# Kernel tuning notes

Measured on AMD Instinct MI355X. Metric: run time of the kernel, lower is better.

## Reference

```python
import jax, jax.numpy as jnp
import numpy as np
from jax import lax

B_SZ, SEQ, D_MODEL, D_STATE, DT_RANK = 4, 4096, 256, 16, 16


def setup_inputs() -> dict:
    key = jax.random.key(0)
    ks = jax.random.split(key, 12)
    d, n, r = D_MODEL, D_STATE, DT_RANK
    inp = {}
    inp["hidden_states"] = jax.random.normal(ks[0], (B_SZ, SEQ, d), jnp.float32)
    inp["in_proj_w"] = jax.random.normal(ks[1], (3 * d, d), jnp.float32) * (d ** -0.5)
    inp["x_proj_w"] = jax.random.normal(ks[2], (r + 2 * n, d), jnp.float32) * (d ** -0.5)
    s = r ** -0.5
    inp["dt_proj_w"] = jax.random.uniform(ks[3], (d, r), jnp.float32, -s, s)
    dt = jnp.exp(jax.random.uniform(ks[4], (d,), jnp.float32) * (np.log(0.1) - np.log(1e-3)) + np.log(1e-3))
    inp["dt_proj_b"] = dt + jnp.log(-jnp.expm1(-dt))  # inverse-softplus init
    inp["A_log"] = jnp.log(jnp.broadcast_to(jnp.arange(1, n + 1, dtype=jnp.float32), (d, n)))
    inp["D"] = jnp.ones((d,), jnp.float32)
    inp["out_proj1_w"] = jax.random.normal(ks[5], (d, d), jnp.float32) * (d ** -0.5)
    inp["conv_x_w"] = jax.random.normal(ks[6], (d, 1, 1), jnp.float32)
    inp["conv_x_b"] = jax.random.normal(ks[7], (d,), jnp.float32) * 0.1
    inp["conv_y_w"] = jax.random.normal(ks[8], (d, 1, 3), jnp.float32) * (3 ** -0.5)
    inp["conv_y_b"] = jax.random.normal(ks[9], (d,), jnp.float32) * 0.1
    inp["conv_z_w"] = jax.random.normal(ks[10], (d, 1, 5), jnp.float32) * (5 ** -0.5)
    inp["conv_z_b"] = jax.random.normal(ks[11], (d,), jnp.float32) * 0.1
    return inp


def _silu(x):
    return x * jax.nn.sigmoid(x)


def _dwconv(x, w, b):
    # x: (b, d, l); w: (d, 1, k) depthwise; 'same' padding (odd k)
    k = w.shape[-1]
    pad = (k - 1) // 2
    out = lax.conv_general_dilated(
        x, w, window_strides=(1,), padding=[(pad, pad)],
        dimension_numbers=("NCH", "OIH", "NCH"), feature_group_count=x.shape[1])
    return out + b[None, :, None]


def _selective_scan(u, delta, A, B, C, D, delta_bias):
    # u, delta: (b,d,l); A: (d,n); B,C: (b,n,l); D, delta_bias: (d,)
    delta = jax.nn.softplus(delta + delta_bias[None, :, None])
    dA = jnp.exp(jnp.einsum("bdl,dn->lbdn", delta, A))          # (l,b,d,n)
    dBu = jnp.einsum("bdl,bnl,bdl->lbdn", delta, B, u)           # (l,b,d,n)
    Ct = jnp.transpose(C, (2, 0, 1))                             # (l,b,n)

    def step(h, inp):
        dA_t, dBu_t, C_t = inp
        h = dA_t * h + dBu_t                                     # (b,d,n)
        y = jnp.einsum("bdn,bn->bd", h, C_t)
        return h, y

    h0 = jnp.zeros(u.shape[:2] + (A.shape[1],), u.dtype)
    _, ys = lax.scan(step, h0, (dA, dBu, Ct))                    # ys: (l,b,d)
    y = jnp.transpose(ys, (1, 2, 0))                             # (b,d,l)
    return y + D[None, :, None] * u


def reference(hidden_states, in_proj_w, x_proj_w, dt_proj_w, dt_proj_b, A_log, D,
              out_proj1_w, conv_x_w, conv_x_b, conv_y_w, conv_y_b, conv_z_w, conv_z_b):
    b, l, d = hidden_states.shape
    xyz = jnp.einsum("ble,de->bdl", hidden_states, in_proj_w)    # (b, 3d, l)
    x, y, z = jnp.split(xyz, 3, axis=1)                          # each (b,d,l)
    A = -jnp.exp(A_log.astype(jnp.float32))
    x = _silu(_dwconv(x, conv_x_w, conv_x_b))
    y = _silu(_dwconv(y, conv_y_w, conv_y_b))
    z = _silu(_dwconv(z, conv_z_w, conv_z_b))
    x_dbl = jnp.einsum("bdl,ed->ble", x, x_proj_w)               # (b,l,r+2n)
    dt_r, Bm, Cm = jnp.split(x_dbl, [DT_RANK, DT_RANK + D_STATE], axis=-1)
    # dt_proj applies bias here; selective_scan adds delta_bias again (faithful to source)
    dt = jnp.einsum("blr,dr->bdl", dt_r, dt_proj_w) + dt_proj_b[None, :, None]
    Bm = jnp.transpose(Bm, (0, 2, 1))                            # (b,n,l)
    Cm = jnp.transpose(Cm, (0, 2, 1))
    p = _selective_scan(x, dt, A, Bm, Cm, D.astype(jnp.float32), dt_proj_b.astype(jnp.float32))
    p = jnp.transpose(p, (0, 2, 1))                              # (b,l,d)
    y = jnp.transpose(y, (0, 2, 1))
    z = jnp.transpose(z, (0, 2, 1))
    l1 = jnp.einsum("bld,ed->ble", p * y, out_proj1_w)
    l2 = l1 * z
    l2 = _dwconv(jnp.transpose(l2, (0, 2, 1)), conv_x_w, conv_x_b)
    return jnp.transpose(l2, (0, 2, 1))                          # (b,l,d)
```

## Files before the change

kernel.cpp:

```cpp
#include <hip/hip_runtime.h>
#include <hip/hip_bf16.h>
#include <math.h>

typedef __hip_bfloat16 bf16;
typedef __attribute__((ext_vector_type(8))) short bf16x8;
typedef __attribute__((ext_vector_type(4))) float f32x4;

#define B_SZ 4
#define SEQ  4096
#define DM   256
#define NST  16
#define NCHK 64
#define LC   (SEQ/NCHK)
#define MT   (B_SZ*SEQ)
#define CT   4
#define NLIN (B_SZ*16*256)

__device__ __forceinline__ float silu_f(float v){ return v / (1.f + __expf(-v)); }
__device__ __forceinline__ float softplus_f(float v){
  return (v > 15.f) ? v : __logf(1.f + __expf(v));
}
__device__ __forceinline__ short f2bf(float f){
  union { bf16 h; short s; } u; u.h = __float2bfloat16(f); return u.s;
}
__device__ __forceinline__ float bf2f(short s){
  union { unsigned int i; float f; } v;
  v.i = ((unsigned int)(unsigned short)s) << 16; return v.f;
}
__device__ __forceinline__ float4 bf4_to_f4(uint2 q){
  float4 f;
  f.x = bf2f((short)(q.x & 0xffffu)); f.y = bf2f((short)(q.x >> 16));
  f.z = bf2f((short)(q.y & 0xffffu)); f.w = bf2f((short)(q.y >> 16));
  return f;
}
__device__ __forceinline__ short4 f4_to_bf4(float4 f){
  short4 s; s.x = f2bf(f.x); s.y = f2bf(f.y); s.z = f2bf(f.z); s.w = f2bf(f.w);
  return s;
}

__device__ __forceinline__ void async_cp16(const short* g, short* l){
  __builtin_amdgcn_global_load_lds(
      (const __attribute__((address_space(1))) unsigned int*)g,
      (__attribute__((address_space(3))) unsigned int*)l, 16, 0, 0);
}

template<int CTRL>
__device__ __forceinline__ float dpp_add_step(float v){
  int x = __builtin_amdgcn_update_dpp(0, __float_as_int(v), CTRL, 0xf, 0xf, true);
  return v + __int_as_float(x);
}

__global__ __launch_bounds__(256)
void cvt_in_k(const float* __restrict__ w_in, const float* __restrict__ w_o1,
              const float* __restrict__ hs,
              short* __restrict__ w_in_b, short* __restrict__ w_o1_b,
              short* __restrict__ hsb)
{
  int i = blockIdx.x * 256 + threadIdx.x;
  if (i < 49152) {
    float4 q = *(const float4*)&w_in[i * 4];
    *(short4*)&w_in_b[i * 4] = f4_to_bf4(q);
  } else if (i < 65536) {
    int j = i - 49152;
    float4 q = *(const float4*)&w_o1[j * 4];
    *(short4*)&w_o1_b[j * 4] = f4_to_bf4(q);
  } else {
    int j = i - 65536;
    float4 q = *(const float4*)&hs[(size_t)j * 4];
    *(short4*)&hsb[(size_t)j * 4] = f4_to_bf4(q);
  }
}

template<int EPI, bool OBF, int BM>
__global__ __launch_bounds__(256)
void mfma_gemm_k(const short* __restrict__ Av, const short* __restrict__ Bw,
                 void* __restrict__ Outv, int N, int K,
                 const float* __restrict__ bias, const short* __restrict__ zc,
                 const float* __restrict__ cwx)
{
  constexpr int BN = 128, BK = 64;
  constexpr int JF = (BM == 64) ? 2 : 4;
  __shared__ short As[BM * BK];
  __shared__ short Bs[BN * BK];
  const int tid  = threadIdx.x;
  const int wave = tid >> 6, lane = tid & 63;
  const int quad = lane >> 4, l16 = lane & 15;
  const int wm = (BM == 64) ? 0 : (wave & 1) * 64;
  const int wn = (BM == 64) ? wave * 32 : (wave >> 1) * 64;
  const int m0 = blockIdx.x * BM, n0 = blockIdx.y * BN;

  f32x4 acc[4][JF] = {};

  for (int k0 = 0; k0 < K; k0 += BK) {
    #pragma unroll
    for (int p = 0; p < BM * 8 / 256; p++) {
      int id = p * 256 + tid;
      int row = id >> 3, slot = id & 7;
      int gch = slot ^ (row & 7);
      async_cp16(Av + (size_t)(m0 + row) * K + k0 + gch * 8,
                 &As[row * 64 + slot * 8]);
    }
    #pragma unroll
    for (int p = 0; p < 4; p++) {
      int id = p * 256 + tid;
      int row = id >> 3, slot = id & 7;
      int gch = slot ^ (row & 7);
      async_cp16(Bw + (size_t)(n0 + row) * K + k0 + gch * 8,
                 &Bs[row * 64 + slot * 8]);
    }
    __syncthreads();
    #pragma unroll
    for (int ks = 0; ks < 2; ks++) {
      bf16x8 fa[4], fb[JF];
      int sa = (ks * 4 + quad) ^ (l16 & 7);
      #pragma unroll
      for (int i = 0; i < 4; i++)
        fa[i] = *(const bf16x8*)&As[(wm + i * 16 + l16) * 64 + sa * 8];
      #pragma unroll
      for (int j = 0; j < JF; j++)
        fb[j] = *(const bf16x8*)&Bs[(wn + j * 16 + l16) * 64 + sa * 8];
      #pragma unroll
      for (int i = 0; i < 4; i++)
        #pragma unroll
        for (int j = 0; j < JF; j++)
          acc[i][j] = __builtin_amdgcn_mfma_f32_16x16x32_bf16(fa[i], fb[j], acc[i][j], 0, 0, 0);
    }
    __syncthreads();
  }

  #pragma unroll
  for (int i = 0; i < 4; i++) {
    #pragma unroll
    for (int j = 0; j < JF; j++) {
      int n = n0 + wn + j * 16 + l16;
      #pragma unroll
      for (int r = 0; r < 4; r++) {
        int m = m0 + wm + i * 16 + quad * 4 + r;
        float v = acc[i][j][r];
        if constexpr (EPI == 2)
          v = v * bf2f(zc[(size_t)m * N + n]) * cwx[n] + bias[n];
        if constexpr (OBF) ((short*)Outv)[(size_t)m * N + n] = f2bf(v);
        else               ((float*)Outv)[(size_t)m * N + n] = v;
      }
    }
  }
}

__global__ __launch_bounds__(256)
void gemm34_k(const short* __restrict__ xcb,
              const float* __restrict__ Bw,
              const float* __restrict__ wdt,
              const float* __restrict__ bdt,
              float* __restrict__ xdbl,
              float* __restrict__ dtv)
{
  constexpr int TM = 32, TK = 16, NN = 48;
  __shared__ __align__(16) float As[TK][TM + 4];
  __shared__ __align__(16) float Bs[TK][64 + 4];
  __shared__ __align__(16) float dt_s[TM][20];
  __shared__ __align__(16) float wdt_s[256][20];
  const int tid = threadIdx.x;
  const int tn = tid & 15, tm = tid >> 4;
  const int m0 = blockIdx.x * TM;
  float acc[2][4] = {};
  const int mlA = tid >> 3, kdA = (tid & 7) * 2;
  const int mlB = tid >> 2, kqB = (tid & 3) * 4;

  {
    float4 q0 = *(const float4*)&wdt[tid * 16 + 0];
    float4 q1 = *(const float4*)&wdt[tid * 16 + 4];
    float4 q2 = *(const float4*)&wdt[tid * 16 + 8];
    float4 q3 = *(const float4*)&wdt[tid * 16 + 12];
    *(float4*)&wdt_s[tid][0]  = q0;
    *(float4*)&wdt_s[tid][4]  = q1;
    *(float4*)&wdt_s[tid][8]  = q2;
    *(float4*)&wdt_s[tid][12] = q3;
  }

  for (int k0 = 0; k0 < 256; k0 += TK) {
    {
      size_t off = (size_t)(m0 + mlA) * 256 + k0 + kdA;
      unsigned int v = *(const unsigned int*)(xcb + off);
      As[kdA + 0][mlA] = bf2f((short)(v & 0xffffu));
      As[kdA + 1][mlA] = bf2f((short)(v >> 16));
    }
    {
      float v0 = 0.f, v1 = 0.f, v2 = 0.f, v3 = 0.f;
      if (mlB < NN) {
        float4 q = *(const float4*)(Bw + (size_t)mlB * 256 + k0 + kqB);
        v0 = q.x; v1 = q.y; v2 = q.z; v3 = q.w;
      }
      Bs[kqB+0][mlB] = v0; Bs[kqB+1][mlB] = v1; Bs[kqB+2][mlB] = v2; Bs[kqB+3][mlB] = v3;
    }
    __syncthreads();
    #pragma unroll
    for (int k = 0; k < TK; k++) {
      float2 av = *(const float2*)&As[k][tm << 1];
      float4 bv = *(const float4*)&Bs[k][tn << 2];
      float a[2] = {av.x, av.y};
      float b[4] = {bv.x, bv.y, bv.z, bv.w};
      #pragma unroll
      for (int i = 0; i < 2; i++)
        #pragma unroll
        for (int j = 0; j < 4; j++)
          acc[i][j] = fmaf(a[i], b[j], acc[i][j]);
    }
    __syncthreads();
  }

  #pragma unroll
  for (int i = 0; i < 2; i++) {
    int m = m0 + (tm << 1) + i;
    #pragma unroll
    for (int j = 0; j < 4; j++) {
      int n = (tn << 2) + j;
      float v = acc[i][j];
      if (n < NN) xdbl[(size_t)m * NN + n] = v;
      if (tn < 4) dt_s[(tm << 1) + i][n] = v;
    }
  }
  __syncthreads();

  const int c0 = tid & 63, rg = tid >> 6;
  float w[4][16];
  float bb[4];
  #pragma unroll
  for (int cc = 0; cc < 4; cc++) {
    int col = cc * 64 + c0;
    #pragma unroll
    for (int q = 0; q < 4; q++) {
      float4 t = *(const float4*)&wdt_s[col][q * 4];
      w[cc][q*4+0] = t.x; w[cc][q*4+1] = t.y; w[cc][q*4+2] = t.z; w[cc][q*4+3] = t.w;
    }
    bb[cc] = 2.f * bdt[col];
  }
  #pragma unroll
  for (int rr = 0; rr < 8; rr++) {
    int row = rg * 8 + rr;
    float dr[16];
    #pragma unroll
    for (int q = 0; q < 4; q++) {
      float4 t = *(const float4*)&dt_s[row][q * 4];
      dr[q*4+0] = t.x; dr[q*4+1] = t.y; dr[q*4+2] = t.z; dr[q*4+3] = t.w;
    }
    #pragma unroll
    for (int cc = 0; cc < 4; cc++) {
      float s = bb[cc];
      #pragma unroll
      for (int k = 0; k < 16; k++) s = fmaf(dr[k], w[cc][k], s);
      dtv[(size_t)(m0 + row) * 256 + cc * 64 + c0] = softplus_f(s);
    }
  }
}

__global__ __launch_bounds__(256)
void conv_silu_k(const short* __restrict__ xyzb,
                 const float* __restrict__ wx, const float* __restrict__ bx,
                 const float* __restrict__ wy, const float* __restrict__ by,
                 const float* __restrict__ wz, const float* __restrict__ bz,
                 short* __restrict__ xcb, short* __restrict__ ycb,
                 short* __restrict__ zcb)
{
  int idx = blockIdx.x * 256 + threadIdx.x;
  int c4 = idx % 192;
  int lt = idx / 192;
  int row0 = lt * CT;
  int l0 = row0 & (SEQ - 1);

  float4 win[CT + 4];
  #pragma unroll
  for (int i = 0; i < CT + 4; i++) {
    int l = l0 + i - 2;
    if (l >= 0 && l < SEQ)
      win[i] = bf4_to_f4(*(const uint2*)(xyzb + (size_t)(row0 + i - 2) * 768 + c4 * 4));
    else
      win[i] = make_float4(0.f, 0.f, 0.f, 0.f);
  }

  if (c4 < 64) {
    int d = c4 * 4;
    float4 w  = *(const float4*)&wx[d];
    float4 bb = *(const float4*)&bx[d];
    #pragma unroll
    for (int t = 0; t < CT; t++) {
      float4 v = win[t + 2], o;
      o.x = silu_f(fmaf(v.x, w.x, bb.x));
      o.y = silu_f(fmaf(v.y, w.y, bb.y));
      o.z = silu_f(fmaf(v.z, w.z, bb.z));
      o.w = silu_f(fmaf(v.w, w.w, bb.w));
      *(short4*)&xcb[(size_t)(row0 + t) * 256 + d] = f4_to_bf4(o);
    }
  } else if (c4 < 128) {
    int d = (c4 - 64) * 4;
    float wq[4][3];
    #pragma unroll
    for (int q = 0; q < 4; q++)
      #pragma unroll
      for (int j = 0; j < 3; j++) wq[q][j] = wy[(d + q) * 3 + j];
    float4 bb = *(const float4*)&by[d];
    #pragma unroll
    for (int t = 0; t < CT; t++) {
      float a0 = bb.x, a1 = bb.y, a2 = bb.z, a3 = bb.w;
      #pragma unroll
      for (int j = 0; j < 3; j++) {
        float4 v = win[t + 1 + j];
        a0 = fmaf(v.x, wq[0][j], a0);
        a1 = fmaf(v.y, wq[1][j], a1);
        a2 = fmaf(v.z, wq[2][j], a2);
        a3 = fmaf(v.w, wq[3][j], a3);
      }
      float4 o; o.x = silu_f(a0); o.y = silu_f(a1); o.z = silu_f(a2); o.w = silu_f(a3);
      *(short4*)&ycb[(size_t)(row0 + t) * 256 + d] = f4_to_bf4(o);
    }
  } else {
    int d = (c4 - 128) * 4;
    float wq[4][5];
    #pragma unroll
    for (int q = 0; q < 4; q++)
      #pragma unroll
      for (int j = 0; j < 5; j++) wq[q][j] = wz[(d + q) * 5 + j];
    float4 bb = *(const float4*)&bz[d];
    #pragma unroll
    for (int t = 0; t < CT; t++) {
      float a0 = bb.x, a1 = bb.y, a2 = bb.z, a3 = bb.w;
      #pragma unroll
      for (int j = 0; j < 5; j++) {
        float4 v = win[t + j];
        a0 = fmaf(v.x, wq[0][j], a0);
        a1 = fmaf(v.y, wq[1][j], a1);
        a2 = fmaf(v.z, wq[2][j], a2);
        a3 = fmaf(v.w, wq[3][j], a3);
      }
      float4 o; o.x = silu_f(a0); o.y = silu_f(a1); o.z = silu_f(a2); o.w = silu_f(a3);
      *(short4*)&zcb[(size_t)(row0 + t) * 256 + d] = f4_to_bf4(o);
    }
  }
}

template<bool PASSC>
__global__ __launch_bounds__(256)
void scan_k(const short* __restrict__ xcb,
            const float* __restrict__ dtv,
            const float* __restrict__ xdbl,
            const float* __restrict__ A_log,
            const float* __restrict__ Dp,
            const float* __restrict__ Hstart,
            float* __restrict__ Pbuf, float* __restrict__ hfbuf,
            const short* __restrict__ ycb,
            short* __restrict__ poutb)
{
  __shared__ __align__(16) float2 du2_s[16 * 66];
  __shared__ __align__(16) float2 BC_s [PASSC ? 16 * 66 : 2];
  __shared__ __align__(16) float  Bc_s [PASSC ? 4 : 16 * 68];
  __shared__ __align__(16) float  y_s  [PASSC ? 16 * 68 : 4];
  const int tid = threadIdx.x;
  const int n = tid & 15, dl = tid >> 4;
  const int ch = blockIdx.x;
  const int d0 = blockIdx.y * 16;
  const int b  = blockIdx.z;
  const int d  = d0 + dl;
  const int t0 = ch * LC;
  const size_t brow = (size_t)b * SEQ;
  const size_t cidx = (size_t)ch * NLIN + ((size_t)b * 16 + blockIdx.y) * 256 + tid;

  float u_r[4];
  #pragma unroll
  for (int i = 0; i < 4; i++) {
    int t = (tid >> 4) + i * 16;
    int dd = tid & 15;
    size_t row = brow + t0 + t;
    float uval = bf2f(xcb[row * 256 + d0 + dd]);
    float dval = dtv[row * 256 + d0 + dd];
    du2_s[dd * 66 + t] = make_float2(dval, dval * uval);
    if constexpr (PASSC) {
      BC_s[dd * 66 + t] = make_float2(xdbl[row * 48 + 16 + dd],
                                      xdbl[row * 48 + 32 + dd]);
      u_r[i] = uval;
    } else {
      Bc_s[dd * 68 + t] = xdbl[row * 48 + 16 + dd];
    }
  }
  __syncthreads();

  const float A_dn = -__expf(A_log[d * NST + n]);

  float h = PASSC ? Hstart[cidx] : 0.f;
  float P = 1.f;
  for (int t4 = 0; t4 < LC; t4 += 4) {
    float4 a = *(const float4*)&du2_s[dl * 66 + t4];
    float4 c = *(const float4*)&du2_s[dl * 66 + t4 + 2];
    float dA[4], du[4];
    dA[0] = __expf(a.x * A_dn); du[0] = a.y;
    dA[1] = __expf(a.z * A_dn); du[1] = a.w;
    dA[2] = __expf(c.x * A_dn); du[2] = c.y;
    dA[3] = __expf(c.z * A_dn); du[3] = c.w;
    if constexpr (!PASSC) {
      float4 f = *(const float4*)&Bc_s[n * 68 + t4];
      float Bv[4] = {f.x, f.y, f.z, f.w};
      #pragma unroll
      for (int j = 0; j < 4; j++) {
        h = fmaf(dA[j], h, du[j] * Bv[j]);
        P *= dA[j];
      }
    } else {
      float4 e = *(const float4*)&BC_s[n * 66 + t4];
      float4 g = *(const float4*)&BC_s[n * 66 + t4 + 2];
      float Bv[4] = {e.x, e.z, g.x, g.z};
      float Cv[4] = {e.y, e.w, g.y, g.w};
      float yv[4];
      #pragma unroll
      for (int j = 0; j < 4; j++) {
        h = fmaf(dA[j], h, du[j] * Bv[j]);
        yv[j] = h * Cv[j];
      }
      #pragma unroll
      for (int j = 0; j < 4; j++) yv[j] = dpp_add_step<0x118>(yv[j]);
      #pragma unroll
      for (int j = 0; j < 4; j++) yv[j] = dpp_add_step<0x114>(yv[j]);
      #pragma unroll
      for (int j = 0; j < 4; j++) yv[j] = dpp_add_step<0x112>(yv[j]);
      #pragma unroll
      for (int j = 0; j < 4; j++) yv[j] = dpp_add_step<0x111>(yv[j]);
      if (n == 15)
        *(float4*)&y_s[dl * 68 + t4] = make_float4(yv[0], yv[1], yv[2], yv[3]);
    }
  }

  if constexpr (!PASSC) {
    Pbuf[cidx] = P;
    hfbuf[cidx] = h;
  } else {
    __syncthreads();
    const float Dval = Dp[d0 + n];
    #pragma unroll
    for (int i = 0; i < 4; i++) {
      int t = (tid >> 4) + i * 16;
      size_t row = brow + t0 + t;
      float p = fmaf(Dval, u_r[i], y_s[n * 68 + t]);
      float yg = bf2f(ycb[row * 256 + d0 + n]);
      poutb[row * 256 + d0 + n] = f2bf(p * yg);
    }
  }
}

__global__ __launch_bounds__(256)
void scan_mid_k(const float* __restrict__ Pbuf, const float* __restrict__ hfbuf,
                float* __restrict__ Hstart)
{
  int lin = blockIdx.x * 256 + threadIdx.x;
  float H = 0.f;
  for (int c = 0; c < NCHK; c++) {
    size_t idx = (size_t)c * NLIN + lin;
    Hstart[idx] = H;
    H = Pbuf[idx] * H + hfbuf[idx];
  }
}

extern "C" void kernel_launch(void* const* d_in, const int* in_sizes, int n_in,
                              void* d_out, int out_size, void* d_ws, size_t ws_size,
                              hipStream_t stream)
{
  const float* hs    = (const float*)d_in[0];
  const float* w_in  = (const float*)d_in[1];
  const float* w_xp  = (const float*)d_in[2];
  const float* w_dt  = (const float*)d_in[3];
  const float* b_dt  = (const float*)d_in[4];
  const float* A_log = (const float*)d_in[5];
  const float* Dp    = (const float*)d_in[6];
  const float* w_o1  = (const float*)d_in[7];
  const float* cwx   = (const float*)d_in[8];
  const float* cbx   = (const float*)d_in[9];
  const float* cwy   = (const float*)d_in[10];
  const float* cby   = (const float*)d_in[11];
  const float* cwz   = (const float*)d_in[12];
  const float* cbz   = (const float*)d_in[13];

  char* wsb = (char*)d_ws;
  short* xyzb = (short*)wsb;
  short* xcb  = (short*)(wsb + (size_t)MT * 768 * 2);
  short* ycb  = xcb + (size_t)MT * 256;
  short* zcb  = ycb + (size_t)MT * 256;
  short* pbufb= zcb + (size_t)MT * 256;
  short* w_in_b = pbufb + (size_t)MT * 256;
  short* w_o1_b = w_in_b + 768 * 256;
  short* hsb  = w_o1_b + 256 * 256;
  float* xdbl = (float*)(hsb + (size_t)MT * 256 + 128);
  float* dtv  = xdbl + (size_t)MT * 48;
  float* Pb   = dtv  + (size_t)MT * 256;
  float* hf   = Pb   + (size_t)NCHK * NLIN;
  float* Hs   = hf   + (size_t)NCHK * NLIN;

  dim3 blk(256);

  cvt_in_k<<<dim3(4352), blk, 0, stream>>>(w_in, w_o1, hs, w_in_b, w_o1_b, hsb);

  mfma_gemm_k<0, true, 64><<<dim3(MT / 64, 768 / 128), blk, 0, stream>>>(
      hsb, w_in_b, xyzb, 768, 256, nullptr, nullptr, nullptr);

  conv_silu_k<<<dim3((MT / CT) * 192 / 256), blk, 0, stream>>>(
      xyzb, cwx, cbx, cwy, cby, cwz, cbz, xcb, ycb, zcb);

  gemm34_k<<<dim3(MT / 32), blk, 0, stream>>>(
      xcb, w_xp, w_dt, b_dt, xdbl, dtv);

  scan_k<false><<<dim3(NCHK, DM / 16, B_SZ), blk, 0, stream>>>(
      xcb, dtv, xdbl, A_log, Dp, nullptr, Pb, hf, nullptr, nullptr);
  scan_mid_k<<<dim3(NLIN / 256), blk, 0, stream>>>(Pb, hf, Hs);
  scan_k<true><<<dim3(NCHK, DM / 16, B_SZ), blk, 0, stream>>>(
      xcb, dtv, xdbl, A_log, Dp, Hs, nullptr, nullptr, ycb, pbufb);

  mfma_gemm_k<2, false, 64><<<dim3(MT / 64, 256 / 128), blk, 0, stream>>>(
      pbufb, w_o1_b, d_out, 256, 256, cbx, zcb, cwx);
}
```

Before: 196.6 us.

## Fuse in-projection GEMM with depthwise conv and SiLU epilogue using halo rows

Replaces the separate in_proj GEMM and conv_silu kernels with one kernel that computes an 80-row tile (64 rows plus 8-row halos on each side), transposes the result through shared memory, and applies the 1/3/5-tap depthwise convolutions with SiLU before writing x, y and z. This removes the bf16 round trip of the 768-wide xyz intermediate through global memory and one kernel launch. In exchange the GEMM recomputes the halo rows, about 25% extra MFMA work, and the epilogue adds register pressure.

```diff
diff --git a/kernel.cpp b/kernel.cpp
--- a/kernel.cpp
+++ b/kernel.cpp
@@ -13,7 +13,6 @@
 #define NCHK 64
 #define LC   (SEQ/NCHK)
 #define MT   (B_SZ*SEQ)
-#define CT   4
 #define NLIN (B_SZ*16*256)
 
 __device__ __forceinline__ float silu_f(float v){ return v / (1.f + __expf(-v)); }
@@ -71,6 +70,151 @@
   }
 }
 
+__global__ __launch_bounds__(256)
+void mfma_gemm_conv_k(const short* __restrict__ Av,
+                      const short* __restrict__ Bw,
+                      const float* __restrict__ wx, const float* __restrict__ bx,
+                      const float* __restrict__ wy, const float* __restrict__ by,
+                      const float* __restrict__ wz, const float* __restrict__ bz,
+                      short* __restrict__ xout, short* __restrict__ yout,
+                      short* __restrict__ zout)
+{
+  constexpr int RM = 80;
+  __shared__ __align__(16) char smem_c[26624];
+  short* As = (short*)smem_c;
+  short* Bs = (short*)(smem_c + 10240);
+  const int tid  = threadIdx.x;
+  const int wave = tid >> 6, lane = tid & 63;
+  const int quad = lane >> 4, l16 = lane & 15;
+  const int wn = wave * 32;
+  const int m0 = blockIdx.x * 64, n0 = blockIdx.y * 128;
+
+  f32x4 acc[5][2] = {};
+
+  for (int k0 = 0; k0 < 256; k0 += 64) {
+    #pragma unroll
+    for (int p = 0; p < 3; p++) {
+      int id = p * 256 + tid;
+      if (id < RM * 8) {
+        int row = id >> 3, slot = id & 7;
+        int gch = slot ^ (row & 7);
+        int gm = m0 - 8 + row;
+        gm = gm < 0 ? 0 : (gm > MT - 1 ? MT - 1 : gm);
+        async_cp16(Av + (size_t)gm * 256 + k0 + gch * 8,
+                   &As[row * 64 + slot * 8]);
+      }
+    }
+    #pragma unroll
+    for (int p = 0; p < 4; p++) {
+      int id = p * 256 + tid;
+      int row = id >> 3, slot = id & 7;
+      int gch = slot ^ (row & 7);
+      async_cp16(Bw + (size_t)(n0 + row) * 256 + k0 + gch * 8,
+                 &Bs[row * 64 + slot * 8]);
+    }
+    __syncthreads();
+    #pragma unroll
+    for (int ks = 0; ks < 2; ks++) {
+      bf16x8 fa[5], fb[2];
+      int sa = (ks * 4 + quad) ^ (l16 & 7);
+      #pragma unroll
+      for (int i = 0; i < 5; i++)
+        fa[i] = *(const bf16x8*)&As[(i * 16 + l16) * 64 + sa * 8];
+      #pragma unroll
+      for (int j = 0; j < 2; j++)
+        fb[j] = *(const bf16x8*)&Bs[(wn + j * 16 + l16) * 64 + sa * 8];
+      #pragma unroll
+      for (int i = 0; i < 5; i++)
+        #pragma unroll
+        for (int j = 0; j < 2; j++)
+          acc[i][j] = __builtin_amdgcn_mfma_f32_16x16x32_bf16(fa[i], fb[j], acc[i][j], 0, 0, 0);
+    }
+    __syncthreads();
+  }
+
+  short* Ts = (short*)smem_c;
+  #pragma unroll
+  for (int i = 0; i < 5; i++) {
+    #pragma unroll
+    for (int j = 0; j < 2; j++) {
+      int col = wn + j * 16 + l16;
+      int row = i * 16 + quad * 4;
+      short4 v;
+      v.x = f2bf(acc[i][j][0]); v.y = f2bf(acc[i][j][1]);
+      v.z = f2bf(acc[i][j][2]); v.w = f2bf(acc[i][j][3]);
+      *(short4*)&Ts[col * 84 + row] = v;
+    }
+  }
+  __syncthreads();
+
+  const int cp = tid & 63, rg = tid >> 6;
+  const int lc0 = cp * 2;
+  const int lr0 = rg * 16;
+  const int lbase = (m0 & (SEQ - 1)) + lr0;
+  float ta[24], tb[24];
+  {
+    const short* q0 = &Ts[lc0 * 84 + lr0 + 4];
+    #pragma unroll
+    for (int q = 0; q < 6; q++) {
+      short4 a = *(const short4*)&q0[q * 4];
+      short4 b = *(const short4*)&q0[84 + q * 4];
+      ta[q*4+0] = bf2f(a.x); ta[q*4+1] = bf2f(a.y);
+      ta[q*4+2] = bf2f(a.z); ta[q*4+3] = bf2f(a.w);
+      tb[q*4+0] = bf2f(b.x); tb[q*4+1] = bf2f(b.y);
+      tb[q*4+2] = bf2f(b.z); tb[q*4+3] = bf2f(b.w);
+    }
+  }
+  const int type = n0 >> 8;
+  const int gq = n0 + lc0 - type * 256;
+  if (type == 0) {
+    float w0 = wx[gq], w1 = wx[gq + 1];
+    float b0 = bx[gq], b1 = bx[gq + 1];
+    #pragma unroll
+    for (int t = 0; t < 16; t++) {
+      short2 o;
+      o.x = f2bf(silu_f(fmaf(ta[t + 4], w0, b0)));
+      o.y = f2bf(silu_f(fmaf(tb[t + 4], w1, b1)));
+      *(short2*)&xout[(size_t)(m0 + lr0 + t) * 256 + gq] = o;
+    }
+  } else if (type == 1) {
+    float w0[3], w1[3];
+    #pragma unroll
+    for (int j = 0; j < 3; j++) { w0[j] = wy[gq*3 + j]; w1[j] = wy[(gq+1)*3 + j]; }
+    float b0 = by[gq], b1 = by[gq + 1];
+    #pragma unroll
+    for (int t = 0; t < 16; t++) {
+      float a0 = b0, a1 = b1;
+      #pragma unroll
+      for (int j = 0; j < 3; j++) {
+        int l = lbase + t + j - 1;
+        bool ok = ((unsigned)l < SEQ);
+        a0 = fmaf(ok ? ta[t + 3 + j] : 0.f, w0[j], a0);
+        a1 = fmaf(ok ? tb[t + 3 + j] : 0.f, w1[j], a1);
+      }
+      short2 o; o.x = f2bf(silu_f(a0)); o.y = f2bf(silu_f(a1));
+      *(short2*)&yout[(size_t)(m0 + lr0 + t) * 256 + gq] = o;
+    }
+  } else {
+    float w0[5], w1[5];
+    #pragma unroll
+    for (int j = 0; j < 5; j++) { w0[j] = wz[gq*5 + j]; w1[j] = wz[(gq+1)*5 + j]; }
+    float b0 = bz[gq], b1 = bz[gq + 1];
+    #pragma unroll
+    for (int t = 0; t < 16; t++) {
+      float a0 = b0, a1 = b1;
+      #pragma unroll
+      for (int j = 0; j < 5; j++) {
+        int l = lbase + t + j - 2;
+        bool ok = ((unsigned)l < SEQ);
+        a0 = fmaf(ok ? ta[t + 2 + j] : 0.f, w0[j], a0);
+        a1 = fmaf(ok ? tb[t + 2 + j] : 0.f, w1[j], a1);
+      }
+      short2 o; o.x = f2bf(silu_f(a0)); o.y = f2bf(silu_f(a1));
+      *(short2*)&zout[(size_t)(m0 + lr0 + t) * 256 + gq] = o;
+    }
+  }
+}
+
 template<int EPI, bool OBF, int BM>
 __global__ __launch_bounds__(256)
 void mfma_gemm_k(const short* __restrict__ Av, const short* __restrict__ Bw,
@@ -249,90 +393,6 @@
       #pragma unroll
       for (int k = 0; k < 16; k++) s = fmaf(dr[k], w[cc][k], s);
       dtv[(size_t)(m0 + row) * 256 + cc * 64 + c0] = softplus_f(s);
-    }
-  }
-}
-
-__global__ __launch_bounds__(256)
-void conv_silu_k(const short* __restrict__ xyzb,
-                 const float* __restrict__ wx, const float* __restrict__ bx,
-                 const float* __restrict__ wy, const float* __restrict__ by,
-                 const float* __restrict__ wz, const float* __restrict__ bz,
-                 short* __restrict__ xcb, short* __restrict__ ycb,
-                 short* __restrict__ zcb)
-{
-  int idx = blockIdx.x * 256 + threadIdx.x;
-  int c4 = idx % 192;
-  int lt = idx / 192;
-  int row0 = lt * CT;
-  int l0 = row0 & (SEQ - 1);
-
-  float4 win[CT + 4];
-  #pragma unroll
-  for (int i = 0; i < CT + 4; i++) {
-    int l = l0 + i - 2;
-    if (l >= 0 && l < SEQ)
-      win[i] = bf4_to_f4(*(const uint2*)(xyzb + (size_t)(row0 + i - 2) * 768 + c4 * 4));
-    else
-      win[i] = make_float4(0.f, 0.f, 0.f, 0.f);
-  }
-
-  if (c4 < 64) {
-    int d = c4 * 4;
-    float4 w  = *(const float4*)&wx[d];
-    float4 bb = *(const float4*)&bx[d];
-    #pragma unroll
-    for (int t = 0; t < CT; t++) {
-      float4 v = win[t + 2], o;
-      o.x = silu_f(fmaf(v.x, w.x, bb.x));
-      o.y = silu_f(fmaf(v.y, w.y, bb.y));
-      o.z = silu_f(fmaf(v.z, w.z, bb.z));
-      o.w = silu_f(fmaf(v.w, w.w, bb.w));
-      *(short4*)&xcb[(size_t)(row0 + t) * 256 + d] = f4_to_bf4(o);
-    }
-  } else if (c4 < 128) {
-    int d = (c4 - 64) * 4;
-    float wq[4][3];
-    #pragma unroll
-    for (int q = 0; q < 4; q++)
-      #pragma unroll
-      for (int j = 0; j < 3; j++) wq[q][j] = wy[(d + q) * 3 + j];
-    float4 bb = *(const float4*)&by[d];
-    #pragma unroll
-    for (int t = 0; t < CT; t++) {
-      float a0 = bb.x, a1 = bb.y, a2 = bb.z, a3 = bb.w;
-      #pragma unroll
-      for (int j = 0; j < 3; j++) {
-        float4 v = win[t + 1 + j];
-        a0 = fmaf(v.x, wq[0][j], a0);
-        a1 = fmaf(v.y, wq[1][j], a1);
-        a2 = fmaf(v.z, wq[2][j], a2);
-        a3 = fmaf(v.w, wq[3][j], a3);
-      }
-      float4 o; o.x = silu_f(a0); o.y = silu_f(a1); o.z = silu_f(a2); o.w = silu_f(a3);
-      *(short4*)&ycb[(size_t)(row0 + t) * 256 + d] = f4_to_bf4(o);
-    }
-  } else {
-    int d = (c4 - 128) * 4;
-    float wq[4][5];
-    #pragma unroll
-    for (int q = 0; q < 4; q++)
-      #pragma unroll
-      for (int j = 0; j < 5; j++) wq[q][j] = wz[(d + q) * 5 + j];
-    float4 bb = *(const float4*)&bz[d];
-    #pragma unroll
-    for (int t = 0; t < CT; t++) {
-      float a0 = bb.x, a1 = bb.y, a2 = bb.z, a3 = bb.w;
-      #pragma unroll
-      for (int j = 0; j < 5; j++) {
-        float4 v = win[t + j];
-        a0 = fmaf(v.x, wq[0][j], a0);
-        a1 = fmaf(v.y, wq[1][j], a1);
-        a2 = fmaf(v.z, wq[2][j], a2);
-        a3 = fmaf(v.w, wq[3][j], a3);
-      }
-      float4 o; o.x = silu_f(a0); o.y = silu_f(a1); o.z = silu_f(a2); o.w = silu_f(a3);
-      *(short4*)&zcb[(size_t)(row0 + t) * 256 + d] = f4_to_bf4(o);
     }
   }
 }
@@ -476,8 +536,7 @@
   const float* cbz   = (const float*)d_in[13];
 
   char* wsb = (char*)d_ws;
-  short* xyzb = (short*)wsb;
-  short* xcb  = (short*)(wsb + (size_t)MT * 768 * 2);
+  short* xcb  = (short*)wsb;
   short* ycb  = xcb + (size_t)MT * 256;
   short* zcb  = ycb + (size_t)MT * 256;
   short* pbufb= zcb + (size_t)MT * 256;
@@ -494,11 +553,8 @@
 
   cvt_in_k<<<dim3(4352), blk, 0, stream>>>(w_in, w_o1, hs, w_in_b, w_o1_b, hsb);
 
-  mfma_gemm_k<0, true, 64><<<dim3(MT / 64, 768 / 128), blk, 0, stream>>>(
-      hsb, w_in_b, xyzb, 768, 256, nullptr, nullptr, nullptr);
-
-  conv_silu_k<<<dim3((MT / CT) * 192 / 256), blk, 0, stream>>>(
-      xyzb, cwx, cbx, cwy, cby, cwz, cbz, xcb, ycb, zcb);
+  mfma_gemm_conv_k<<<dim3(MT / 64, 768 / 128), blk, 0, stream>>>(
+      hsb, w_in_b, cwx, cbx, cwy, cby, cwz, cbz, xcb, ycb, zcb);
 
   gemm34_k<<<dim3(MT / 32), blk, 0, stream>>>(
       xcb, w_xp, w_dt, b_dt, xdbl, dtv);
```

Measured after the change: 188.8 us. -3.9%, faster.
